# Optimization experiments

Measured on AMD Instinct MI355X. Metric: run time of the kernel, lower is better.

The kernel has to match this reference:

```python
import jax, jax.numpy as jnp
import numpy as np

DN = ('NCHW', 'OIHW', 'NCHW')
EPS = 1e-5


def _conv(x, w, b, stride, pad):
    y = jax.lax.conv_general_dilated(x, w, (stride, stride), ((pad, pad), (pad, pad)), dimension_numbers=DN)
    return y + b[None, :, None, None]


def _convT(x, w, b):
    # PyTorch ConvTranspose2d(k=3, stride=2, padding=1, output_padding=1)
    # weight w: [in, out, kh, kw] -> flip spatial, swap in/out -> OIHW
    wt = jnp.flip(w, (2, 3)).transpose(1, 0, 2, 3)
    y = jax.lax.conv_general_dilated(x, wt, (1, 1), ((1, 2), (1, 2)), lhs_dilation=(2, 2), dimension_numbers=DN)
    return y + b[None, :, None, None]


def _inorm(x):
    # InstanceNorm2d, affine=False, biased variance (num_features arg unused since no affine)
    m = x.mean((2, 3), keepdims=True)
    v = ((x - m) ** 2).mean((2, 3), keepdims=True)
    return (x - m) / jnp.sqrt(v + EPS)


def _lrelu(x):
    return jnp.where(x >= 0, x, 0.2 * x)


def _refpad(x):
    return jnp.pad(x, ((0, 0), (0, 0), (1, 1), (1, 1)), mode='reflect')


def _backbone(image, w1, b1, w2, b2, w3, b3, wt, bt, w4, b4):
    x = _lrelu(_inorm(_conv(_refpad(image), w1, b1, 1, 0)))   # [B,32,H,W]
    x = _lrelu(_inorm(_conv(x, w2, b2, 2, 1)))                 # [B,64,H/2,W/2]
    x = _lrelu(_inorm(_conv(x, w3, b3, 2, 1)))                 # [B,128,H/4,W/4]
    x = _lrelu(_inorm(_convT(x, wt, bt)))                      # [B,256,H/2,W/2]
    x = jnp.tanh(_conv(_refpad(x), w4, b4, 1, 0))              # [B,512,H/2,W/2]
    return x


def _style_codes(x, seg):
    # nearest interpolation of seg to (h,w): src_idx = floor(dst * H / h)
    B, C, h, w = x.shape
    H, W = seg.shape[2], seg.shape[3]
    rows = (np.arange(h) * H) // h
    cols = (np.arange(w) * W) // w
    seg_ds = seg[:, :, rows][:, :, :, cols]                    # [B,L,h,w]
    m = (seg_ds != 0).astype(x.dtype)
    sums = jnp.einsum('bchw,blhw->blc', x, m)                  # segment sums
    counts = m.sum((2, 3))[..., None]                          # [B,L,1]
    return jnp.where(counts > 0, sums / jnp.maximum(counts, 1.0), 0.0)


def setup_inputs():
    key = jax.random.key(0)
    ks = jax.random.split(key, 8)
    B, H, W, L = 8, 256, 256, 19
    image = jax.random.normal(ks[0], (B, 3, H, W), jnp.float32)
    labels = jax.random.randint(ks[1], (B, H, W), 0, L)
    seg = jax.nn.one_hot(labels, L, axis=1, dtype=jnp.float32)  # one-hot semantic map
    def w(k, shape):
        return jax.random.normal(k, shape, jnp.float32) * 0.05
    return {
        'image': image, 'seg': seg,
        'w1': w(ks[2], (32, 3, 3, 3)), 'b1': jnp.zeros(32, jnp.float32),
        'w2': w(ks[3], (64, 32, 3, 3)), 'b2': jnp.zeros(64, jnp.float32),
        'w3': w(ks[4], (128, 64, 3, 3)), 'b3': jnp.zeros(128, jnp.float32),
        'wt': w(ks[5], (128, 256, 3, 3)), 'bt': jnp.zeros(256, jnp.float32),
        'w4': w(ks[6], (512, 256, 3, 3)), 'b4': jnp.zeros(512, jnp.float32),
    }


def reference(image, seg, w1, b1, w2, b2, w3, b3, wt, bt, w4, b4):
    x = _backbone(image, w1, b1, w2, b2, w3, b3, wt, bt, w4, b4)
    return _style_codes(x, seg)  # [B, label_nc, 512]
```

## Files before the change

### kernel.cpp

```cpp
#include <hip/hip_runtime.h>
#include <hip/hip_bf16.h>
#include <math.h>

typedef __attribute__((ext_vector_type(8))) short bf16x8;
typedef __attribute__((ext_vector_type(8))) unsigned short u16x8;
typedef __attribute__((ext_vector_type(4))) float f32x4;
typedef __attribute__((ext_vector_type(2))) long longx2;

#define OFF_X1   0ull
#define OFF_XQ8  0ull
#define OFF_X2   34080768ull
#define OFF_X3   51386368ull
#define OFF_Y4   60039168ull
#define OFF_WB8  127148032ull
#define OFF_WB2  129507328ull
#define OFF_WB3  129548288ull
#define OFF_WBT  129695744ull
#define OFF_ST1  130744320ull
#define OFF_ST2  130746368ull
#define OFF_ST3  130750464ull
#define OFF_ST4  130758656ull
#define OFF_SUMS 130775040ull
#define OFF_CNT  131086336ull
#define OFF_MS1  131086944ull
#define OFF_MS2  131088992ull
#define OFF_MS3  131093088ull
#define OFF_MS4  131101280ull
#define OFF_LAB  131117664ull
#define OFF_DWS  131641952ull
#define OFF_WSM  132166240ull
#define OFF_ST5  132690528ull
#define OFF_CB   132706912ull

__device__ __forceinline__ float bfu2f(unsigned short u) {
  return __builtin_bit_cast(float, ((unsigned)u) << 16);
}
__device__ __forceinline__ unsigned short f2bfu(float f) {
  __hip_bfloat16 h = __float2bfloat16(f);
  return __builtin_bit_cast(unsigned short, h);
}
__device__ __forceinline__ void gload_lds16(const void* g, void* l) {
  __builtin_amdgcn_global_load_lds(
      (const __attribute__((address_space(1))) unsigned int*)g,
      (__attribute__((address_space(3))) unsigned int*)l, 16, 0, 0);
}
template <bool HI>
__device__ __forceinline__ int cvtpk8(float a, float b, int old) {
  return __builtin_amdgcn_cvt_pk_fp8_f32(a, b, old, HI);
}
template <int SEL>
__device__ __forceinline__ float cvtf8(int v) {
  return __builtin_amdgcn_cvt_f32_fp8(v, SEL);
}

#define WAITV(N) asm volatile("s_waitcnt vmcnt(" #N ")" ::: "memory")

#define PIPE_STEP(WAITN, BUF, DOSTAGE, SNEXT)                 \
  asm volatile("s_waitcnt vmcnt(" #WAITN ")" ::: "memory");   \
  __builtin_amdgcn_s_barrier();                               \
  __builtin_amdgcn_sched_barrier(0);                          \
  mmaStep(BUF, (BUF) + 16384);                                \
  __builtin_amdgcn_sched_barrier(0);                          \
  __builtin_amdgcn_s_barrier();                               \
  if (DOSTAGE) stage(SNEXT, BUF);

__device__ const int c_taptab[16] = {4, -1, -1, -1, 5, 3, -1, -1, 7, -1, 1, -1, 8, 6, 2, 0};

__global__ __launch_bounds__(256) void prep_k(
    const float* __restrict__ w2, unsigned short* __restrict__ wb2,
    const float* __restrict__ w3, unsigned short* __restrict__ wb3,
    const float* __restrict__ wt, unsigned short* __restrict__ wbt,
    const float* __restrict__ w4, unsigned char* __restrict__ wb8,
    float* __restrict__ dws, float* __restrict__ wsum,
    unsigned short* __restrict__ x1, unsigned short* __restrict__ x2,
    unsigned short* __restrict__ x3,
    const float* __restrict__ seg, int* __restrict__ lab, float* __restrict__ counts) {
  __shared__ int hist[19];
  int blk = blockIdx.x, t = threadIdx.x;
  if (blk < 80) {
    int idx = blk * 256 + t;
    if (idx < 20480) {
      int oc = idx / 320, r = idx % 320, tap = r >> 5, ic = r & 31;
      wb2[idx] = tap < 9 ? f2bfu(w2[(oc * 32 + ic) * 9 + tap]) : (unsigned short)0;
    }
  } else if (blk < 368) {
    int idx = (blk - 80) * 256 + t;
    int oc = idx / 576, r = idx % 576, tap = r >> 6, ic = r & 63;
    wb3[idx] = f2bfu(w3[(oc * 64 + ic) * 9 + tap]);
  } else if (blk < 2416) {
    int idx = (blk - 368) * 256 + t;
    int n = idx >> 9, k = idx & 511;
    int cl = n >> 8, oc = n & 255, nb = k >> 7, ic = k & 127;
    int tap = c_taptab[cl * 4 + nb];
    wbt[idx] = tap < 0 ? (unsigned short)0 : f2bfu(wt[(ic * 256 + oc) * 9 + tap]);
  } else if (blk < 2928) {
    int oc = blk - 2416, ic = t;
    int local = ic & 127;
    int p = (ic & 128) + ((local >> 3) & 3) * 32 + ((local >> 5) & 3) * 8 + (local & 7);
    float ds = 0.f, ws = 0.f;
    for (int kk = 0; kk < 9; ++kk) {
      float w = w4[(size_t)oc * 2304 + ic * 9 + kk];
      int pk = cvtpk8<false>(w, 0.f, 0);
      wb8[((size_t)oc * 9 + kk) * 256 + p] = (unsigned char)(pk & 0xff);
      float wq = cvtf8<0>(pk);
      ds += wq - w; ws += w;
    }
    dws[oc * 256 + ic] = ds;
    wsum[oc * 256 + ic] = ws;
  } else if (blk < 3252) {
    int u = (blk - 2928) * 256 + t;
    int b = u / 10368, r = u % 10368;
    u16x8 z = {0, 0, 0, 0, 0, 0, 0, 0};
    if (r < 4128) {
      unsigned short* base = x1 + (size_t)b * 2130048;
      if (r < 2064) {
        int row = r < 1032 ? 0 : 257, pos = r < 1032 ? r : r - 1032;
        base += (row * 258 + (pos >> 2)) * 32 + (pos & 3) * 8;
      } else {
        int rc = r - 2064;
        int col = rc < 1032 ? 0 : 257, pos = rc < 1032 ? rc : rc - 1032;
        base += ((pos >> 2) * 258 + col) * 32 + (pos & 3) * 8;
      }
      *(u16x8*)base = z;
    } else if (r < 8288) {
      int s = r - 4128;
      unsigned short* base = x2 + (size_t)b * 1081600;
      if (s < 2080) {
        int row = s < 1040 ? 0 : 129, pos = s < 1040 ? s : s - 1040;
        base += (row * 130 + (pos >> 3)) * 64 + (pos & 7) * 8;
      } else {
        int sc = s - 2080;
        int col = sc < 1040 ? 0 : 129, pos = sc < 1040 ? sc : sc - 1040;
        base += ((pos >> 3) * 130 + col) * 64 + (pos & 7) * 8;
      }
      *(u16x8*)base = z;
    } else {
      int tt = r - 8288;
      unsigned short* base = x3 + (size_t)b * 540800;
      if (tt < 1040) {
        base += (64 * 65 + (tt >> 4)) * 128 + (tt & 15) * 8;
      } else {
        int pos = tt - 1040;
        base += ((pos >> 4) * 65 + 64) * 128 + (pos & 15) * 8;
      }
      *(u16x8*)base = z;
    }
  } else {
    int blk2 = blk - 3252;
    int b = blk2 >> 6;
    int p = (blk2 & 63) * 256 + t;
    if (t < 19) hist[t] = 0;
    __syncthreads();
    int i = p >> 7, j = p & 127;
    const float* sp = seg + (size_t)b * 19 * 65536 + (2 * i) * 256 + 2 * j;
    int l = 0;
    for (int k = 0; k < 19; ++k) { if (sp[(size_t)k * 65536] != 0.f) { l = k; break; } }
    lab[b * 16384 + p] = l;
    atomicAdd(&hist[l], 1);
    __syncthreads();
    if (t < 19) atomicAdd(&counts[b * 19 + t], (float)hist[t]);
  }
}

__global__ __launch_bounds__(256) void conv1_k(const float* __restrict__ img,
                                               const float* __restrict__ w1,
                                               unsigned short* __restrict__ x1) {
  __shared__ float wl[864];
  int t = threadIdx.x, y = blockIdx.x, b = blockIdx.y;
  for (int i = t; i < 864; i += 256) wl[i] = w1[(i & 31) * 27 + (i >> 5)];
  __syncthreads();
  int x = t;
  float val[27];
  for (int ic = 0; ic < 3; ++ic) {
    const float* ip = img + ((size_t)(b * 3 + ic)) * 65536;
#pragma unroll
    for (int ky = 0; ky < 3; ++ky) {
      int gy = y - 1 + ky; gy = gy < 0 ? -gy : (gy > 255 ? 510 - gy : gy);
#pragma unroll
      for (int kx = 0; kx < 3; ++kx) {
        int gx = x - 1 + kx; gx = gx < 0 ? -gx : (gx > 255 ? 510 - gx : gx);
        val[ic * 9 + ky * 3 + kx] = ip[gy * 256 + gx];
      }
    }
  }
  float a[32];
#pragma unroll
  for (int oc = 0; oc < 32; ++oc) a[oc] = 0.f;
#pragma unroll
  for (int k = 0; k < 27; ++k) {
    float vv = val[k];
#pragma unroll
    for (int oc = 0; oc < 32; ++oc) a[oc] += wl[k * 32 + oc] * vv;
  }
  unsigned short ov[32];
#pragma unroll
  for (int oc = 0; oc < 32; ++oc) ov[oc] = f2bfu(a[oc]);
  unsigned short* op = x1 + ((size_t)(b * 258 + y + 1) * 258 + (x + 1)) * 32;
#pragma unroll
  for (int i = 0; i < 4; ++i) *(u16x8*)(op + i * 8) = *(const u16x8*)(ov + i * 8);
}

template <int C>
__global__ void statsn_k(const unsigned short* __restrict__ base, int rowStride, int unitsLog,
                         int rowsPer, long bStride, float* __restrict__ stats) {
  const int CH8 = C / 8;
  __shared__ float bins[C * 2];
  int tid = threadIdx.x, slice = blockIdx.x, b = blockIdx.y;
  for (int i = tid; i < C * 2; i += 256) bins[i] = 0.f;
  __syncthreads();
  const unsigned short* bp = base + (size_t)b * bStride + (size_t)(slice * rowsPer) * rowStride;
  int total = rowsPer << unitsLog;
  float s8[8] = {0, 0, 0, 0, 0, 0, 0, 0}, q8[8] = {0, 0, 0, 0, 0, 0, 0, 0};
  for (int idx = tid; idx < total; idx += 256) {
    int rl = idx >> unitsLog, ux = idx & ((1 << unitsLog) - 1);
    u16x8 v = *(const u16x8*)(bp + (size_t)rl * rowStride + ux * 8);
#pragma unroll
    for (int e = 0; e < 8; ++e) { float f = bfu2f(v[e]); s8[e] += f; q8[e] += f * f; }
  }
#pragma unroll
  for (int e = 0; e < 8; ++e)
    for (int off = 32; off >= CH8; off >>= 1) {
      s8[e] += __shfl_xor(s8[e], off);
      q8[e] += __shfl_xor(q8[e], off);
    }
  int lane = tid & 63;
  if (lane < CH8) {
#pragma unroll
    for (int e = 0; e < 8; ++e) {
      atomicAdd(&bins[(lane * 8 + e) * 2], s8[e]);
      atomicAdd(&bins[(lane * 8 + e) * 2 + 1], q8[e]);
    }
  }
  __syncthreads();
  for (int i = tid; i < C * 2; i += 256) atomicAdd(&stats[b * C * 2 + i], bins[i]);
}

__global__ void msn_k(const float* __restrict__ st, float2* __restrict__ ms, float invN, int total) {
  int i = blockIdx.x * 256 + threadIdx.x;
  if (i < total) {
    float m = st[2 * i] * invN;
    float v = st[2 * i + 1] * invN - m * m;
    ms[i] = make_float2(m, rsqrtf(fmaxf(v, 0.f) + 1e-5f));
  }
}

template <int C>
__global__ void nln_k(unsigned short* __restrict__ base, int rowStride, int unitsPerRow,
                      long bStride, const float2* __restrict__ ms) {
  const int CH8 = C / 8;
  int row = blockIdx.x, b = blockIdx.y;
  unsigned short* rp = base + (size_t)b * bStride + (size_t)row * rowStride;
  const float2* msb = ms + b * C;
  for (int idx = threadIdx.x; idx < unitsPerRow; idx += 256) {
    u16x8 v = *(u16x8*)(rp + idx * 8);
    int ch = (idx & (CH8 - 1)) * 8;
    u16x8 o;
#pragma unroll
    for (int e = 0; e < 8; ++e) {
      float2 m = msb[ch + e];
      float f = (bfu2f(v[e]) - m.x) * m.y;
      o[e] = f2bfu(f >= 0.f ? f : 0.2f * f);
    }
    *(u16x8*)(rp + idx * 8) = o;
  }
}

__global__ __launch_bounds__(256) void nln8_k(const unsigned short* __restrict__ y4,
                                              const float2* __restrict__ ms,
                                              unsigned char* __restrict__ xq8,
                                              float* __restrict__ st5) {
  __shared__ float bs[512];
  int t = threadIdx.x, row = blockIdx.x, b = blockIdx.y;
  int cg = t & 31, pg = t >> 5;
  int wof0 = (cg >> 4) * 128 + ((((cg & 15) & 3) << 2) | ((cg & 15) >> 2)) * 8;
  const float2* msb = ms + b * 256;
  float2 m0[8];
#pragma unroll
  for (int e = 0; e < 8; ++e) m0[e] = msb[cg * 8 + e];
  const unsigned short* rp = y4 + ((size_t)b * 16384 + row * 128) * 256;
  unsigned char* op = xq8 + ((size_t)b * 16384 + (size_t)row * 128) * 256;
  float s[8] = {0, 0, 0, 0, 0, 0, 0, 0}, d[8] = {0, 0, 0, 0, 0, 0, 0, 0};
  for (int i = 0; i < 16; ++i) {
    int px = pg * 16 + i;
    u16x8 v = *(const u16x8*)(rp + (size_t)px * 256 + cg * 8);
    float f[8];
#pragma unroll
    for (int e = 0; e < 8; ++e) {
      float x = (bfu2f(v[e]) - m0[e].x) * m0[e].y;
      f[e] = x >= 0.f ? x : 0.2f * x;
    }
    int lo = cvtpk8<false>(f[0], f[1], 0); lo = cvtpk8<true>(f[2], f[3], lo);
    int hi = cvtpk8<false>(f[4], f[5], 0); hi = cvtpk8<true>(f[6], f[7], hi);
    *(long*)(op + (size_t)px * 256 + wof0) =
        ((long)(unsigned)hi << 32) | (unsigned)lo;
    float fq;
    fq = cvtf8<0>(lo); s[0] += fq; d[0] += fq - f[0];
    fq = cvtf8<1>(lo); s[1] += fq; d[1] += fq - f[1];
    fq = cvtf8<2>(lo); s[2] += fq; d[2] += fq - f[2];
    fq = cvtf8<3>(lo); s[3] += fq; d[3] += fq - f[3];
    fq = cvtf8<0>(hi); s[4] += fq; d[4] += fq - f[4];
    fq = cvtf8<1>(hi); s[5] += fq; d[5] += fq - f[5];
    fq = cvtf8<2>(hi); s[6] += fq; d[6] += fq - f[6];
    fq = cvtf8<3>(hi); s[7] += fq; d[7] += fq - f[7];
  }
  for (int i = t; i < 512; i += 256) bs[i] = 0.f;
  __syncthreads();
#pragma unroll
  for (int e = 0; e < 8; ++e) {
    atomicAdd(&bs[cg * 8 + e], s[e]);
    atomicAdd(&bs[256 + cg * 8 + e], d[e]);
  }
  __syncthreads();
  for (int i = t; i < 512; i += 256) atomicAdd(&st5[b * 512 + i], bs[i]);
}

__global__ __launch_bounds__(256) void cbias_k(const float* __restrict__ st5,
                                               const float* __restrict__ dws,
                                               const float* __restrict__ wsum,
                                               float* __restrict__ cb) {
  int oc = blockIdx.x, b = blockIdx.y, t = threadIdx.x;
  const float inv = 1.f / 16384.f;
  float muq = st5[b * 512 + t] * inv;
  float dmu = st5[b * 512 + 256 + t] * inv;
  float a = muq * dws[oc * 256 + t] + dmu * wsum[oc * 256 + t];
#pragma unroll
  for (int o = 1; o < 64; o <<= 1) a += __shfl_xor(a, o);
  __shared__ float r[4];
  if ((t & 63) == 0) r[t >> 6] = a;
  __syncthreads();
  if (t == 0) cb[b * 512 + oc] = r[0] + r[1] + r[2] + r[3];
}

__global__ __launch_bounds__(256) void conv2_k(const unsigned short* __restrict__ x1,
                                               const unsigned short* __restrict__ wb2,
                                               unsigned short* __restrict__ x2,
                                               float* __restrict__ st2) {
  __shared__ char smem[49664];
  float* bins = (float*)(smem + 49152);
  int tid = threadIdx.x, y = blockIdx.x, b = blockIdx.y;
  int lane = tid & 63, w = tid >> 6, wm = w >> 1, wn = w & 1;
  int lr = lane & 15, lg = lane >> 4;
  f32x4 acc[4][2];
#pragma unroll
  for (int i = 0; i < 4; ++i)
#pragma unroll
    for (int j = 0; j < 2; ++j) acc[i][j] = (f32x4){0.f, 0.f, 0.f, 0.f};

  int rowA[4], lcA[4], PbA[4];
#pragma unroll
  for (int i = 0; i < 4; ++i) {
    int pb = i * 256 + tid;
    PbA[i] = pb * 16; rowA[i] = pb >> 3; lcA[i] = (pb & 7) ^ (rowA[i] & 7);
  }
  int rowB[2], lcB[2], PbB[2];
#pragma unroll
  for (int i = 0; i < 2; ++i) {
    int pb = i * 256 + tid;
    PbB[i] = pb * 16; rowB[i] = pb >> 3; lcB[i] = (pb & 7) ^ (rowB[i] & 7);
  }
  const unsigned short* xb = x1 + (size_t)b * 2130048;

  auto stage = [&](int kb, char* base) {
    char* As = base;
    char* Bs = base + 16384;
#pragma unroll
    for (int i = 0; i < 4; ++i) {
      int tp = kb * 2 + (lcA[i] >> 2);
      int ky = (tp * 11) >> 5;
      int kx = tp - ky * 3;
      gload_lds16(xb + ((size_t)((2 * y + ky) * 258 + 2 * rowA[i] + kx)) * 32 + (lcA[i] & 3) * 8,
                  As + PbA[i]);
    }
#pragma unroll
    for (int i = 0; i < 2; ++i)
      gload_lds16(wb2 + rowB[i] * 320 + kb * 64 + lcB[i] * 8, Bs + PbB[i]);
  };

  stage(0, smem);
  __syncthreads();
  for (int kb = 0; kb < 5; ++kb) {
    char* base = smem + (kb & 1) * 24576;
    if (kb + 1 < 5) stage(kb + 1, smem + ((kb + 1) & 1) * 24576);
    char* As = base;
    char* Bs = base + 16384;
    bf16x8 af[4][2], bfr[2][2];
#pragma unroll
    for (int mi = 0; mi < 4; ++mi)
#pragma unroll
      for (int kh = 0; kh < 2; ++kh) {
        int row = wm * 64 + mi * 16 + lr;
        int byte = row * 128 + ((kh * 64 + lg * 16) ^ ((row & 7) << 4));
        af[mi][kh] = *(const bf16x8*)(As + byte);
      }
#pragma unroll
    for (int ni = 0; ni < 2; ++ni)
#pragma unroll
      for (int kh = 0; kh < 2; ++kh) {
        int row = wn * 32 + ni * 16 + lr;
        int byte = row * 128 + ((kh * 64 + lg * 16) ^ ((row & 7) << 4));
        bfr[ni][kh] = *(const bf16x8*)(Bs + byte);
      }
#pragma unroll
    for (int mi = 0; mi < 4; ++mi)
#pragma unroll
      for (int ni = 0; ni < 2; ++ni)
#pragma unroll
        for (int kh = 0; kh < 2; ++kh)
          acc[mi][ni] = __builtin_amdgcn_mfma_f32_16x16x32_bf16(af[mi][kh], bfr[ni][kh],
                                                                acc[mi][ni], 0, 0, 0);
    __syncthreads();
  }

  if (tid < 128) bins[tid] = 0.f;
  __syncthreads();
  unsigned short* ob = x2 + (size_t)b * 1081600;
#pragma unroll
  for (int ni = 0; ni < 2; ++ni) {
    int oc = wn * 32 + ni * 16 + lr;
    float s = 0.f, q = 0.f;
#pragma unroll
    for (int mi = 0; mi < 4; ++mi)
#pragma unroll
      for (int r = 0; r < 4; ++r) {
        int m = wm * 64 + mi * 16 + lg * 4 + r;
        float v = acc[mi][ni][r];
        ob[((y + 1) * 130 + m + 1) * 64 + oc] = f2bfu(v);
        s += v; q += v * v;
      }
    atomicAdd(&bins[oc * 2], s);
    atomicAdd(&bins[oc * 2 + 1], q);
  }
  __syncthreads();
  if (tid < 128) atomicAdd(&st2[b * 128 + tid], bins[tid]);
}

__global__ __launch_bounds__(256) void conv3_k(const unsigned short* __restrict__ x2,
                                               const unsigned short* __restrict__ wb3,
                                               unsigned short* __restrict__ x3,
                                               float* __restrict__ st3) {
  __shared__ char smem[66560];
  float* bins = (float*)(smem + 65536);
  int tid = threadIdx.x, y0 = blockIdx.x * 2, b = blockIdx.y;
  int lane = tid & 63, w = tid >> 6, wm = w >> 1, wn = w & 1;
  int lr = lane & 15, lg = lane >> 4;
  f32x4 acc[4][4];
#pragma unroll
  for (int i = 0; i < 4; ++i)
#pragma unroll
    for (int j = 0; j < 4; ++j) acc[i][j] = (f32x4){0.f, 0.f, 0.f, 0.f};

  int rowS[4], lc[4], Pb[4];
#pragma unroll
  for (int i = 0; i < 4; ++i) {
    int pb = i * 256 + tid;
    Pb[i] = pb * 16; rowS[i] = pb >> 3; lc[i] = (pb & 7) ^ (rowS[i] & 7);
  }
  const unsigned short* xb = x2 + (size_t)b * 1081600;

  auto stage = [&](int kk, char* base) {
    int ky = kk / 3, kx = kk - ky * 3;
#pragma unroll
    for (int i = 0; i < 4; ++i) {
      int m = rowS[i], di = m >> 6, xx = m & 63;
      gload_lds16(xb + ((size_t)((2 * (y0 + di) + ky) * 130 + 2 * xx + kx)) * 64 + lc[i] * 8,
                  base + Pb[i]);
    }
#pragma unroll
    for (int i = 0; i < 4; ++i)
      gload_lds16(wb3 + (rowS[i] * 9 + kk) * 64 + lc[i] * 8, base + 16384 + Pb[i]);
  };

  stage(0, smem);
  __syncthreads();
  for (int kk = 0; kk < 9; ++kk) {
    char* base = smem + (kk & 1) * 32768;
    if (kk + 1 < 9) stage(kk + 1, smem + ((kk + 1) & 1) * 32768);
    char* As = base;
    char* Bs = base + 16384;
    bf16x8 af[4][2], bfr[4][2];
#pragma unroll
    for (int mi = 0; mi < 4; ++mi)
#pragma unroll
      for (int kh = 0; kh < 2; ++kh) {
        int row = wm * 64 + mi * 16 + lr;
        int byte = row * 128 + ((kh * 64 + lg * 16) ^ ((row & 7) << 4));
        af[mi][kh] = *(const bf16x8*)(As + byte);
      }
#pragma unroll
    for (int ni = 0; ni < 4; ++ni)
#pragma unroll
      for (int kh = 0; kh < 2; ++kh) {
        int row = wn * 64 + ni * 16 + lr;
        int byte = row * 128 + ((kh * 64 + lg * 16) ^ ((row & 7) << 4));
        bfr[ni][kh] = *(const bf16x8*)(Bs + byte);
      }
#pragma unroll
    for (int mi = 0; mi < 4; ++mi)
#pragma unroll
      for (int ni = 0; ni < 4; ++ni)
#pragma unroll
        for (int kh = 0; kh < 2; ++kh)
          acc[mi][ni] = __builtin_amdgcn_mfma_f32_16x16x32_bf16(af[mi][kh], bfr[ni][kh],
                                                                acc[mi][ni], 0, 0, 0);
    __syncthreads();
  }

  if (tid < 256) bins[tid] = 0.f;
  __syncthreads();
  unsigned short* ob = x3 + (size_t)b * 540800;
#pragma unroll
  for (int ni = 0; ni < 4; ++ni) {
    int oc = wn * 64 + ni * 16 + lr;
    float s = 0.f, q = 0.f;
#pragma unroll
    for (int mi = 0; mi < 4; ++mi)
#pragma unroll
      for (int r = 0; r < 4; ++r) {
        int m = wm * 64 + mi * 16 + lg * 4 + r;
        int di = m >> 6, xx = m & 63;
        float v = acc[mi][ni][r];
        ob[((y0 + di) * 65 + xx) * 128 + oc] = f2bfu(v);
        s += v; q += v * v;
      }
    atomicAdd(&bins[oc * 2], s);
    atomicAdd(&bins[oc * 2 + 1], q);
  }
  __syncthreads();
  if (tid < 256) atomicAdd(&st3[b * 256 + tid], bins[tid]);
}

__global__ __launch_bounds__(256) void convT_k(const unsigned short* __restrict__ x3,
                                               const unsigned short* __restrict__ wbt,
                                               unsigned short* __restrict__ y4,
                                               float* __restrict__ st4) {
  __shared__ char smem[67584];
  float* bins = (float*)(smem + 65536);
  int tid = threadIdx.x, i0 = blockIdx.x * 2, nblk = blockIdx.y, b = blockIdx.z;
  int n0 = nblk * 128, cl = nblk >> 1, och0 = (nblk & 1) * 128;
  int lane = tid & 63, w = tid >> 6, wm = w >> 1, wn = w & 1;
  int lr = lane & 15, lg = lane >> 4;
  f32x4 acc[4][4];
#pragma unroll
  for (int i = 0; i < 4; ++i)
#pragma unroll
    for (int j = 0; j < 4; ++j) acc[i][j] = (f32x4){0.f, 0.f, 0.f, 0.f};

  int rowS[4], lc[4], Pb[4];
#pragma unroll
  for (int i = 0; i < 4; ++i) {
    int pb = i * 256 + tid;
    Pb[i] = pb * 16; rowS[i] = pb >> 3; lc[i] = (pb & 7) ^ (rowS[i] & 7);
  }
  int aoff[4][2], boff[4][2];
#pragma unroll
  for (int mi = 0; mi < 4; ++mi)
#pragma unroll
    for (int kh = 0; kh < 2; ++kh) {
      int row = wm * 64 + mi * 16 + lr;
      aoff[mi][kh] = row * 128 + ((kh * 64 + lg * 16) ^ ((row & 7) << 4));
      int rowb = wn * 64 + mi * 16 + lr;
      boff[mi][kh] = rowb * 128 + ((kh * 64 + lg * 16) ^ ((rowb & 7) << 4));
    }
  const unsigned short* xb = x3 + (size_t)b * 540800;

  auto stage = [&](int kb, char* base) {
    int nb = kb >> 1, chalf = (kb & 1) * 64;
#pragma unroll
    for (int i = 0; i < 4; ++i) {
      int m = rowS[i], di = m >> 6, j = m & 63;
      int pi = i0 + di + (nb >> 1), pj = j + (nb & 1);
      gload_lds16(xb + ((size_t)(pi * 65 + pj)) * 128 + chalf + lc[i] * 8, base + Pb[i]);
    }
#pragma unroll
    for (int i = 0; i < 4; ++i)
      gload_lds16(wbt + (size_t)(n0 + rowS[i]) * 512 + kb * 64 + lc[i] * 8,
                  base + 16384 + Pb[i]);
  };

  auto mmaStep = [&](char* As, char* Bs) {
    bf16x8 af[4][2], bfr[4][2];
#pragma unroll
    for (int mi = 0; mi < 4; ++mi)
#pragma unroll
      for (int kh = 0; kh < 2; ++kh) af[mi][kh] = *(const bf16x8*)(As + aoff[mi][kh]);
#pragma unroll
    for (int ni = 0; ni < 4; ++ni)
#pragma unroll
      for (int kh = 0; kh < 2; ++kh) bfr[ni][kh] = *(const bf16x8*)(Bs + boff[ni][kh]);
#pragma unroll
    for (int mi = 0; mi < 4; ++mi)
#pragma unroll
      for (int ni = 0; ni < 4; ++ni)
#pragma unroll
        for (int kh = 0; kh < 2; ++kh)
          acc[mi][ni] = __builtin_amdgcn_mfma_f32_16x16x32_bf16(af[mi][kh], bfr[ni][kh],
                                                                acc[mi][ni], 0, 0, 0);
  };

  char* B0 = smem;
  char* B1 = smem + 32768;
  stage(0, B0);
  stage(1, B1);
  for (int sp = 0; sp < 3; ++sp) {
    PIPE_STEP(8, B0, true, 2 * sp + 2);
    PIPE_STEP(8, B1, true, 2 * sp + 3);
  }
  PIPE_STEP(8, B0, false, 0);
  PIPE_STEP(0, B1, false, 0);

  if (tid < 256) bins[tid] = 0.f;
  __syncthreads();
  unsigned short* ob = y4 + (size_t)b * 4194304;
  int dy = cl >> 1, dx = cl & 1;
#pragma unroll
  for (int ni = 0; ni < 4; ++ni) {
    int loc = wn * 64 + ni * 16 + lr;
    int oc = och0 + loc;
    float s = 0.f, q = 0.f;
#pragma unroll
    for (int mi = 0; mi < 4; ++mi)
#pragma unroll
      for (int r = 0; r < 4; ++r) {
        int m = wm * 64 + mi * 16 + lg * 4 + r;
        int di = m >> 6, j = m & 63;
        int oy = 2 * (i0 + di) + dy, ox = 2 * j + dx;
        float v = acc[mi][ni][r];
        ob[(oy * 128 + ox) * 256 + oc] = f2bfu(v);
        s += v; q += v * v;
      }
    atomicAdd(&bins[loc * 2], s);
    atomicAdd(&bins[loc * 2 + 1], q);
  }
  __syncthreads();
  if (tid < 256) atomicAdd(&st4[b * 512 + och0 * 2 + tid], bins[tid]);
}

__global__ __launch_bounds__(256, 3) void conv4_k(
    const unsigned char* __restrict__ xq8, const unsigned char* __restrict__ wb8,
    const float* __restrict__ b4, const float* __restrict__ cb,
    const int* __restrict__ lab, float* __restrict__ sums) {
  __shared__ char smem[33280];
  char* As = smem;
  char* Bs = smem + 16384;
  int* labs = (int*)(smem + 32768);
  int tid = threadIdx.x;
  int id = blockIdx.x;
  int b = id & 7, rr = id >> 3;
  int y = rr >> 2, nblk = rr & 3;
  int n0 = nblk * 128;
  if (tid < 128) labs[tid] = lab[b * 16384 + y * 128 + tid];
  int lane = tid & 63, w = tid >> 6;
  int wm = w >> 1, wn = w & 1;
  int lr = lane & 15, lg = lane >> 4;

  f32x4 acc[4][4];
#pragma unroll
  for (int i = 0; i < 4; ++i)
#pragma unroll
    for (int j = 0; j < 4; ++j) acc[i][j] = (f32x4){0.f, 0.f, 0.f, 0.f};

  const unsigned char* xb = xq8 + (size_t)b * 4194304;

  int rs0 = tid >> 3;
  int csw = ((tid & 7) ^ (rs0 & 7)) << 4;
  int ldoff = tid * 16;

  const unsigned char* brow[4];
#pragma unroll
  for (int i = 0; i < 4; ++i)
    brow[i] = wb8 + (size_t)(n0 + rs0 + 32 * i) * 2304 + csw;

  int koff = 0;
  for (int kk = 0; kk < 9; ++kk) {
    int ky = (kk * 11) >> 5, kx = kk - ky * 3;
    int sy = y + ky - 1; sy = sy < 0 ? 1 : (sy > 127 ? 126 : sy);
    const unsigned char* arow[4];
#pragma unroll
    for (int i = 0; i < 4; ++i) {
      int sx = rs0 + 32 * i + kx - 1;
      sx = sx < 0 ? 1 : (sx > 127 ? 126 : sx);
      arow[i] = xb + ((size_t)(sy * 128 + sx)) * 256 + csw;
    }
    for (int ic0 = 0; ic0 < 256; ic0 += 128) {
      __syncthreads();
#pragma unroll
      for (int i = 0; i < 4; ++i) gload_lds16(arow[i] + ic0, As + i * 4096 + ldoff);
#pragma unroll
      for (int i = 0; i < 4; ++i) gload_lds16(brow[i] + koff, Bs + i * 4096 + ldoff);
      koff += 128;
      __syncthreads();

      longx2 bq[4][2];
#pragma unroll
      for (int ni = 0; ni < 4; ++ni) {
        int row = wn * 64 + ni * 16 + lr;
#pragma unroll
        for (int k2 = 0; k2 < 2; ++k2) {
          int byte = row * 128 + ((lg * 32 + k2 * 16) ^ ((row & 7) << 4));
          bq[ni][k2] = *(const longx2*)(Bs + byte);
        }
      }
#pragma unroll
      for (int mi = 0; mi < 4; ++mi) {
        int row = wm * 64 + mi * 16 + lr;
        longx2 aq[2];
#pragma unroll
        for (int k2 = 0; k2 < 2; ++k2) {
          int byte = row * 128 + ((lg * 32 + k2 * 16) ^ ((row & 7) << 4));
          aq[k2] = *(const longx2*)(As + byte);
        }
#pragma unroll
        for (int ni = 0; ni < 4; ++ni)
#pragma unroll
          for (int k2 = 0; k2 < 2; ++k2) {
            acc[mi][ni] = __builtin_amdgcn_mfma_f32_16x16x32_fp8_fp8(
                aq[k2][0], bq[ni][k2][0], acc[mi][ni], 0, 0, 0);
            acc[mi][ni] = __builtin_amdgcn_mfma_f32_16x16x32_fp8_fp8(
                aq[k2][1], bq[ni][k2][1], acc[mi][ni], 0, 0, 0);
          }
      }
    }
  }

  __syncthreads();
  float* bins = (float*)smem;
  for (int t2 = tid; t2 < 19 * 128; t2 += 256) bins[t2] = 0.f;
  __syncthreads();
  float bias[4];
#pragma unroll
  for (int ni = 0; ni < 4; ++ni) {
    int gc = n0 + wn * 64 + ni * 16 + lr;
    bias[ni] = b4[gc] - cb[b * 512 + gc];
  }
#pragma unroll
  for (int mi = 0; mi < 4; ++mi)
#pragma unroll
    for (int ni = 0; ni < 4; ++ni) {
      int ct = wn * 64 + ni * 16 + lr;
#pragma unroll
      for (int r = 0; r < 4; ++r) {
        int x = wm * 64 + mi * 16 + lg * 4 + r;
        float v = tanhf(acc[mi][ni][r] + bias[ni]);
        atomicAdd(&bins[labs[x] * 128 + ct], v);
      }
    }
  __syncthreads();
  for (int t2 = tid; t2 < 19 * 128; t2 += 256) {
    float v = bins[t2];
    if (v != 0.f)
      atomicAdd(&sums[((size_t)(b * 19 + (t2 >> 7))) * 512 + n0 + (t2 & 127)], v);
  }
}

__global__ void finalize_k(const float* __restrict__ sums, const float* __restrict__ counts,
                           float* __restrict__ out) {
  int idx = blockIdx.x * 256 + threadIdx.x;
  int bl = idx / 512;
  float c = counts[bl];
  out[idx] = c > 0.f ? sums[idx] / fmaxf(c, 1.f) : 0.f;
}

extern "C" void kernel_launch(void* const* d_in, const int* in_sizes, int n_in,
                              void* d_out, int out_size, void* d_ws, size_t ws_size,
                              hipStream_t stream) {
  const float* image = (const float*)d_in[0];
  const float* seg   = (const float*)d_in[1];
  const float* w1    = (const float*)d_in[2];
  const float* w2    = (const float*)d_in[4];
  const float* w3    = (const float*)d_in[6];
  const float* wt    = (const float*)d_in[8];
  const float* w4    = (const float*)d_in[10];
  const float* b4    = (const float*)d_in[11];
  float* out = (float*)d_out;
  char* ws = (char*)d_ws;

  unsigned short* x1  = (unsigned short*)(ws + OFF_X1);
  unsigned char*  xq8 = (unsigned char*)(ws + OFF_XQ8);
  unsigned short* x2  = (unsigned short*)(ws + OFF_X2);
  unsigned short* x3  = (unsigned short*)(ws + OFF_X3);
  unsigned short* y4  = (unsigned short*)(ws + OFF_Y4);
  unsigned char*  wb8 = (unsigned char*)(ws + OFF_WB8);
  unsigned short* wb2 = (unsigned short*)(ws + OFF_WB2);
  unsigned short* wb3 = (unsigned short*)(ws + OFF_WB3);
  unsigned short* wbt = (unsigned short*)(ws + OFF_WBT);
  float* st1 = (float*)(ws + OFF_ST1);
  float* st2 = (float*)(ws + OFF_ST2);
  float* st3 = (float*)(ws + OFF_ST3);
  float* st4 = (float*)(ws + OFF_ST4);
  float* sums = (float*)(ws + OFF_SUMS);
  float* counts = (float*)(ws + OFF_CNT);
  float2* ms1 = (float2*)(ws + OFF_MS1);
  float2* ms2 = (float2*)(ws + OFF_MS2);
  float2* ms3 = (float2*)(ws + OFF_MS3);
  float2* ms4 = (float2*)(ws + OFF_MS4);
  int* lab = (int*)(ws + OFF_LAB);
  float* dws  = (float*)(ws + OFF_DWS);
  float* wsum = (float*)(ws + OFF_WSM);
  float* st5  = (float*)(ws + OFF_ST5);
  float* cbv  = (float*)(ws + OFF_CB);

  hipMemsetAsync(ws + OFF_ST1, 0, 342624, stream);
  hipMemsetAsync(ws + OFF_ST5, 0, 16384, stream);
  prep_k<<<3764, 256, 0, stream>>>(w2, wb2, w3, wb3, wt, wbt, w4, wb8, dws, wsum,
                                   x1, x2, x3, seg, lab, counts);

  conv1_k<<<dim3(256, 8), 256, 0, stream>>>(image, w1, x1);
  statsn_k<32><<<dim3(16, 8), 256, 0, stream>>>(x1 + 259 * 32, 258 * 32, 10, 16, 2130048L, st1);
  msn_k<<<1, 256, 0, stream>>>(st1, ms1, 1.f / 65536.f, 256);
  nln_k<32><<<dim3(256, 8), 256, 0, stream>>>(x1 + 259 * 32, 258 * 32, 1024, 2130048L, ms1);

  conv2_k<<<dim3(128, 8), 256, 0, stream>>>(x1, wb2, x2, st2);
  msn_k<<<2, 256, 0, stream>>>(st2, ms2, 1.f / 16384.f, 512);
  nln_k<64><<<dim3(128, 8), 256, 0, stream>>>(x2 + 131 * 64, 130 * 64, 1024, 1081600L, ms2);

  conv3_k<<<dim3(32, 8), 256, 0, stream>>>(x2, wb3, x3, st3);
  msn_k<<<4, 256, 0, stream>>>(st3, ms3, 1.f / 4096.f, 1024);
  nln_k<128><<<dim3(64, 8), 256, 0, stream>>>(x3, 65 * 128, 1024, 540800L, ms3);

  convT_k<<<dim3(32, 8, 8), 256, 0, stream>>>(x3, wbt, y4, st4);
  msn_k<<<8, 256, 0, stream>>>(st4, ms4, 1.f / 16384.f, 2048);

  nln8_k<<<dim3(128, 8), 256, 0, stream>>>(y4, ms4, xq8, st5);
  cbias_k<<<dim3(512, 8), 256, 0, stream>>>(st5, dws, wsum, cbv);

  conv4_k<<<4096, 256, 0, stream>>>(xq8, wb8, b4, cbv, lab, sums);

  finalize_k<<<304, 256, 0, stream>>>(sums, counts, out);
}
```

Before: 720.9 us.

## Fuse conv1 instance-norm stats into conv1 and fold mean/rstd into normalize kernels

conv1 now reduces per-channel sum and sum-of-squares through a shared-memory tile transpose and accumulates them into st1. This removes the separate statsn pass that re-read the whole bf16 x1 tensor. The four msn_k launches are also removed: each normalize kernel (nln_k, nln8_k) now computes mean and rstd for its own channels directly from the raw stats. The cost is extra shared memory and a reduction phase in conv1, plus redundant per-block rsqrt work. Stats for layer 1 are now taken from fp32 accumulators rather than bf16-rounded values.

Result: faster. 696.7 us (-3.4%).

```diff
diff --git a/kernel.cpp b/kernel.cpp
--- a/kernel.cpp
+++ b/kernel.cpp
@@ -22,10 +22,6 @@
 #define OFF_ST4  130758656ull
 #define OFF_SUMS 130775040ull
 #define OFF_CNT  131086336ull
-#define OFF_MS1  131086944ull
-#define OFF_MS2  131088992ull
-#define OFF_MS3  131093088ull
-#define OFF_MS4  131101280ull
 #define OFF_LAB  131117664ull
 #define OFF_DWS  131641952ull
 #define OFF_WSM  132166240ull
@@ -164,10 +160,14 @@
 
 __global__ __launch_bounds__(256) void conv1_k(const float* __restrict__ img,
                                                const float* __restrict__ w1,
-                                               unsigned short* __restrict__ x1) {
+                                               unsigned short* __restrict__ x1,
+                                               float* __restrict__ st1) {
   __shared__ float wl[864];
+  __shared__ float tile[256][33];
+  __shared__ float cbins[64];
   int t = threadIdx.x, y = blockIdx.x, b = blockIdx.y;
   for (int i = t; i < 864; i += 256) wl[i] = w1[(i & 31) * 27 + (i >> 5)];
+  if (t < 64) cbins[t] = 0.f;
   __syncthreads();
   int x = t;
   float val[27];
@@ -198,67 +198,43 @@
   unsigned short* op = x1 + ((size_t)(b * 258 + y + 1) * 258 + (x + 1)) * 32;
 #pragma unroll
   for (int i = 0; i < 4; ++i) *(u16x8*)(op + i * 8) = *(const u16x8*)(ov + i * 8);
-}
-
-template <int C>
-__global__ void statsn_k(const unsigned short* __restrict__ base, int rowStride, int unitsLog,
-                         int rowsPer, long bStride, float* __restrict__ stats) {
-  const int CH8 = C / 8;
-  __shared__ float bins[C * 2];
-  int tid = threadIdx.x, slice = blockIdx.x, b = blockIdx.y;
-  for (int i = tid; i < C * 2; i += 256) bins[i] = 0.f;
-  __syncthreads();
-  const unsigned short* bp = base + (size_t)b * bStride + (size_t)(slice * rowsPer) * rowStride;
-  int total = rowsPer << unitsLog;
-  float s8[8] = {0, 0, 0, 0, 0, 0, 0, 0}, q8[8] = {0, 0, 0, 0, 0, 0, 0, 0};
-  for (int idx = tid; idx < total; idx += 256) {
-    int rl = idx >> unitsLog, ux = idx & ((1 << unitsLog) - 1);
-    u16x8 v = *(const u16x8*)(bp + (size_t)rl * rowStride + ux * 8);
-#pragma unroll
-    for (int e = 0; e < 8; ++e) { float f = bfu2f(v[e]); s8[e] += f; q8[e] += f * f; }
-  }
-#pragma unroll
-  for (int e = 0; e < 8; ++e)
-    for (int off = 32; off >= CH8; off >>= 1) {
-      s8[e] += __shfl_xor(s8[e], off);
-      q8[e] += __shfl_xor(q8[e], off);
-    }
-  int lane = tid & 63;
-  if (lane < CH8) {
-#pragma unroll
-    for (int e = 0; e < 8; ++e) {
-      atomicAdd(&bins[(lane * 8 + e) * 2], s8[e]);
-      atomicAdd(&bins[(lane * 8 + e) * 2 + 1], q8[e]);
-    }
-  }
-  __syncthreads();
-  for (int i = tid; i < C * 2; i += 256) atomicAdd(&stats[b * C * 2 + i], bins[i]);
-}
-
-__global__ void msn_k(const float* __restrict__ st, float2* __restrict__ ms, float invN, int total) {
-  int i = blockIdx.x * 256 + threadIdx.x;
-  if (i < total) {
-    float m = st[2 * i] * invN;
-    float v = st[2 * i + 1] * invN - m * m;
-    ms[i] = make_float2(m, rsqrtf(fmaxf(v, 0.f) + 1e-5f));
-  }
+
+#pragma unroll
+  for (int oc = 0; oc < 32; ++oc) tile[t][oc] = a[oc];
+  __syncthreads();
+  int ch = t & 31, seg = t >> 5;
+  float s = 0.f, q = 0.f;
+  for (int r = 0; r < 32; ++r) {
+    float v = tile[seg * 32 + ((r + seg) & 31)][ch];
+    s += v; q += v * v;
+  }
+  atomicAdd(&cbins[ch * 2], s);
+  atomicAdd(&cbins[ch * 2 + 1], q);
+  __syncthreads();
+  if (t < 64) atomicAdd(&st1[b * 64 + t], cbins[t]);
 }
 
 template <int C>
 __global__ void nln_k(unsigned short* __restrict__ base, int rowStride, int unitsPerRow,
-                      long bStride, const float2* __restrict__ ms) {
+                      long bStride, const float* __restrict__ st, float invN) {
   const int CH8 = C / 8;
   int row = blockIdx.x, b = blockIdx.y;
   unsigned short* rp = base + (size_t)b * bStride + (size_t)row * rowStride;
-  const float2* msb = ms + b * C;
+  int ch = (threadIdx.x & (CH8 - 1)) * 8;
+  const float* stb = st + b * C * 2;
+  float2 m0[8];
+#pragma unroll
+  for (int e = 0; e < 8; ++e) {
+    float m = stb[(ch + e) * 2] * invN;
+    float v = stb[(ch + e) * 2 + 1] * invN - m * m;
+    m0[e] = make_float2(m, rsqrtf(fmaxf(v, 0.f) + 1e-5f));
+  }
   for (int idx = threadIdx.x; idx < unitsPerRow; idx += 256) {
     u16x8 v = *(u16x8*)(rp + idx * 8);
-    int ch = (idx & (CH8 - 1)) * 8;
     u16x8 o;
 #pragma unroll
     for (int e = 0; e < 8; ++e) {
-      float2 m = msb[ch + e];
-      float f = (bfu2f(v[e]) - m.x) * m.y;
+      float f = (bfu2f(v[e]) - m0[e].x) * m0[e].y;
       o[e] = f2bfu(f >= 0.f ? f : 0.2f * f);
     }
     *(u16x8*)(rp + idx * 8) = o;
@@ -266,17 +242,22 @@
 }
 
 __global__ __launch_bounds__(256) void nln8_k(const unsigned short* __restrict__ y4,
-                                              const float2* __restrict__ ms,
+                                              const float* __restrict__ st4,
                                               unsigned char* __restrict__ xq8,
                                               float* __restrict__ st5) {
   __shared__ float bs[512];
   int t = threadIdx.x, row = blockIdx.x, b = blockIdx.y;
   int cg = t & 31, pg = t >> 5;
   int wof0 = (cg >> 4) * 128 + ((((cg & 15) & 3) << 2) | ((cg & 15) >> 2)) * 8;
-  const float2* msb = ms + b * 256;
+  const float* stb = st4 + b * 512;
+  const float invN = 1.f / 16384.f;
   float2 m0[8];
 #pragma unroll
-  for (int e = 0; e < 8; ++e) m0[e] = msb[cg * 8 + e];
+  for (int e = 0; e < 8; ++e) {
+    float m = stb[(cg * 8 + e) * 2] * invN;
+    float v = stb[(cg * 8 + e) * 2 + 1] * invN - m * m;
+    m0[e] = make_float2(m, rsqrtf(fmaxf(v, 0.f) + 1e-5f));
+  }
   const unsigned short* rp = y4 + ((size_t)b * 16384 + row * 128) * 256;
   unsigned char* op = xq8 + ((size_t)b * 16384 + (size_t)row * 128) * 256;
   float s[8] = {0, 0, 0, 0, 0, 0, 0, 0}, d[8] = {0, 0, 0, 0, 0, 0, 0, 0};
@@ -789,10 +770,6 @@
   float* st4 = (float*)(ws + OFF_ST4);
   float* sums = (float*)(ws + OFF_SUMS);
   float* counts = (float*)(ws + OFF_CNT);
-  float2* ms1 = (float2*)(ws + OFF_MS1);
-  float2* ms2 = (float2*)(ws + OFF_MS2);
-  float2* ms3 = (float2*)(ws + OFF_MS3);
-  float2* ms4 = (float2*)(ws + OFF_MS4);
   int* lab = (int*)(ws + OFF_LAB);
   float* dws  = (float*)(ws + OFF_DWS);
   float* wsum = (float*)(ws + OFF_WSM);
@@ -804,23 +781,21 @@
   prep_k<<<3764, 256, 0, stream>>>(w2, wb2, w3, wb3, wt, wbt, w4, wb8, dws, wsum,
                                    x1, x2, x3, seg, lab, counts);
 
-  conv1_k<<<dim3(256, 8), 256, 0, stream>>>(image, w1, x1);
-  statsn_k<32><<<dim3(16, 8), 256, 0, stream>>>(x1 + 259 * 32, 258 * 32, 10, 16, 2130048L, st1);
-  msn_k<<<1, 256, 0, stream>>>(st1, ms1, 1.f / 65536.f, 256);
-  nln_k<32><<<dim3(256, 8), 256, 0, stream>>>(x1 + 259 * 32, 258 * 32, 1024, 2130048L, ms1);
+  conv1_k<<<dim3(256, 8), 256, 0, stream>>>(image, w1, x1, st1);
+  nln_k<32><<<dim3(256, 8), 256, 0, stream>>>(x1 + 259 * 32, 258 * 32, 1024, 2130048L,
+                                              st1, 1.f / 65536.f);
 
   conv2_k<<<dim3(128, 8), 256, 0, stream>>>(x1, wb2, x2, st2);
-  msn_k<<<2, 256, 0, stream>>>(st2, ms2, 1.f / 16384.f, 512);
-  nln_k<64><<<dim3(128, 8), 256, 0, stream>>>(x2 + 131 * 64, 130 * 64, 1024, 1081600L, ms2);
+  nln_k<64><<<dim3(128, 8), 256, 0, stream>>>(x2 + 131 * 64, 130 * 64, 1024, 1081600L,
+                                              st2, 1.f / 16384.f);
 
   conv3_k<<<dim3(32, 8), 256, 0, stream>>>(x2, wb3, x3, st3);
-  msn_k<<<4, 256, 0, stream>>>(st3, ms3, 1.f / 4096.f, 1024);
-  nln_k<128><<<dim3(64, 8), 256, 0, stream>>>(x3, 65 * 128, 1024, 540800L, ms3);
+  nln_k<128><<<dim3(64, 8), 256, 0, stream>>>(x3, 65 * 128, 1024, 540800L,
+                                              st3, 1.f / 4096.f);
 
   convT_k<<<dim3(32, 8, 8), 256, 0, stream>>>(x3, wbt, y4, st4);
-  msn_k<<<8, 256, 0, stream>>>(st4, ms4, 1.f / 16384.f, 2048);
-
-  nln8_k<<<dim3(128, 8), 256, 0, stream>>>(y4, ms4, xq8, st5);
+
+  nln8_k<<<dim3(128, 8), 256, 0, stream>>>(y4, st4, xq8, st5);
   cbias_k<<<dim3(512, 8), 256, 0, stream>>>(st5, dws, wsum, cbv);
 
   conv4_k<<<4096, 256, 0, stream>>>(xq8, wb8, b4, cbv, lab, sums);
```
